# Optimization experiments

Hardware: AMD Instinct MI355X
Metric: run time of the kernel (lower is better)

Reference implementation:

```python
import jax, jax.numpy as jnp
import numpy as np

EPS = 1e-5      # BatchNorm eps (eval mode, running stats at init: mean=0, var=1)
SLOPE = 0.2     # LeakyReLU negative slope


def _knn_idx(x, k):
    # x: (B, N, D) -> (B, N, k) indices of k nearest neighbors (squared L2, feature space)
    sq = jnp.sum(x * x, axis=-1)                              # (B, N)
    dist = sq[:, :, None] + sq[:, None, :] - 2.0 * jnp.einsum('bnd,bmd->bnm', x, x)
    return jax.lax.top_k(-dist, k)[1]                         # nearest = largest of -dist


def _bn_lrelu(y, gamma, beta):
    # eval BatchNorm with running_mean=0, running_var=1, then LeakyReLU(0.2)
    y = y * (gamma / jnp.sqrt(1.0 + EPS)) + beta
    return jnp.where(y >= 0, y, SLOPE * y)


def _edge_conv(x, W, gamma, beta, k):
    # x: (B, N, D); W: (C_out, 2D). Returns (B, N, C_out) after max over k neighbors.
    idx = _knn_idx(x, k)                                      # (B, N, k)
    nb = jax.vmap(lambda xt, i: xt[i])(x, idx)                # (B, N, k, D) neighbor gather
    ctr = jnp.broadcast_to(x[:, :, None, :], nb.shape)
    feat = jnp.concatenate([nb - ctr, ctr], axis=-1)          # (B, N, k, 2D)
    y = jnp.einsum('bnkd,od->bnko', feat, W)                  # 1x1 conv (no bias)
    y = _bn_lrelu(y, gamma, beta)
    return jnp.max(y, axis=2)                                 # max-pool over neighbors


def setup_inputs() -> dict:
    key = jax.random.key(0)
    ks = jax.random.split(key, 16)
    B, N, k, out_dim = 8, 4096, 20, 512
    x = jax.random.normal(ks[0], (B, 3, N), dtype=jnp.float32)
    dims = [(64, 6), (64, 128), (128, 128), (256, 256), (out_dim, 512)]
    inp = {'x': x, 'k': k}
    for i, (co, ci) in enumerate(dims, start=1):
        inp[f'W{i}'] = jax.random.normal(ks[3 * i - 2], (co, ci), dtype=jnp.float32) * (1.0 / np.sqrt(ci))
        inp[f'g{i}'] = jax.random.uniform(ks[3 * i - 1], (co,), dtype=jnp.float32, minval=0.5, maxval=1.5)
        inp[f'b{i}'] = 0.1 * jax.random.normal(ks[3 * i], (co,), dtype=jnp.float32)
    return inp


def reference(x, W1, g1, b1, W2, g2, b2, W3, g3, b3, W4, g4, b4, W5, g5, b5, k):
    xt = jnp.transpose(x, (0, 2, 1))                          # (B, N, 3)
    x1 = _edge_conv(xt, W1, g1, b1, k)                        # (B, N, 64)
    x2 = _edge_conv(x1, W2, g2, b2, k)                        # (B, N, 64)
    x3 = _edge_conv(x2, W3, g3, b3, k)                        # (B, N, 128)
    x4 = _edge_conv(x3, W4, g4, b4, k)                        # (B, N, 256)
    h = jnp.concatenate([x1, x2, x3, x4], axis=-1)            # (B, N, 512)
    y = _bn_lrelu(jnp.einsum('bnd,od->bno', h, W5), g5, b5)   # (B, N, out_dim)
    return jnp.concatenate([jnp.max(y, axis=1), jnp.mean(y, axis=1)], axis=-1)  # (B, 2*out_dim)
```

## Files before the change

### kernel.cpp

```cpp
#include <hip/hip_runtime.h>
#include <math.h>

#define BATCH 8
#define N_PTS 4096
#define KNN 20
#define EPS_BN 1e-5f
#define SLOPE 0.2f
#define M_ROWS (BATCH * N_PTS)

typedef __attribute__((ext_vector_type(8))) short short8;
typedef __attribute__((ext_vector_type(2))) float float2v;
typedef __attribute__((ext_vector_type(4))) float float4v;
typedef __attribute__((ext_vector_type(16))) float float16v;

__device__ __forceinline__ unsigned short f2bf(float f) {
    unsigned u = __float_as_uint(f);
    unsigned r = (u + 0x7FFFu + ((u >> 16) & 1u)) >> 16;
    return (unsigned short)r;
}
__device__ __forceinline__ float bf2f(unsigned short h) {
    return __uint_as_float((unsigned)h << 16);
}

__global__ void convert_x1(const float* __restrict__ x,
                           unsigned short* __restrict__ xh, unsigned short* __restrict__ xl,
                           float* __restrict__ sq) {
    int i = blockIdx.x * blockDim.x + threadIdx.x;
    if (i >= M_ROWS) return;
    int b = i / N_PTS, n = i % N_PTS;
    float v[3], s = 0.f;
    #pragma unroll
    for (int d = 0; d < 3; ++d) {
        v[d] = x[((size_t)b * 3 + d) * N_PTS + n];
        s += v[d] * v[d];
    }
    sq[i] = s;
    #pragma unroll
    for (int d = 0; d < 32; ++d) {
        float f = (d < 3) ? v[d] : 0.f;
        unsigned short h = f2bf(f);
        xh[(size_t)i * 32 + d] = h;
        xl[(size_t)i * 32 + d] = f2bf(f - bf2f(h));
    }
}

__global__ void sqnorm_hl(const unsigned short* __restrict__ hh,
                          const unsigned short* __restrict__ hl,
                          int D, float* __restrict__ sq) {
    int w = threadIdx.x >> 6, lane = threadIdx.x & 63;
    int row = blockIdx.x * 4 + w;
    if (row >= M_ROWS) return;
    const unsigned short* ph = hh + (size_t)row * 512;
    const unsigned short* pl = hl + (size_t)row * 512;
    float s = 0.f;
    for (int d = lane; d < D; d += 64) {
        float v = bf2f(ph[d]) + bf2f(pl[d]);
        s += v * v;
    }
    #pragma unroll
    for (int off = 32; off > 0; off >>= 1) s += __shfl_down(s, off, 64);
    if (lane == 0) sq[row] = s;
}

__global__ void repack_edge_split(const float* __restrict__ W, int Co, int D, int KP,
                                  unsigned short* __restrict__ Wh, unsigned short* __restrict__ Wl) {
    int i = blockIdx.x * blockDim.x + threadIdx.x;
    int tot = 2 * Co * KP;
    if (i >= tot) return;
    int r = i / KP, d = i % KP;
    float v = 0.f;
    if (d < D) v = (r < Co) ? W[(size_t)r * 2 * D + d] : W[(size_t)(r - Co) * 2 * D + D + d];
    unsigned short h = f2bf(v);
    Wh[i] = h; Wl[i] = f2bf(v - bf2f(h));
}

__global__ void repack_w5_split(const float* __restrict__ W,
                                unsigned short* __restrict__ Wh, unsigned short* __restrict__ Wl) {
    int i = blockIdx.x * blockDim.x + threadIdx.x;
    if (i >= 512 * 512) return;
    float v = W[i];
    unsigned short h = f2bf(v);
    Wh[i] = h; Wl[i] = f2bf(v - bf2f(h));
}

template<int DPAD>
__launch_bounds__(256, 2)
__global__ void knn_mfma(const unsigned short* __restrict__ Xh,
                         const unsigned short* __restrict__ Xl,
                         int strideX,
                         const float* __restrict__ sq, int* __restrict__ idxout) {
    constexpr int KS16 = DPAD / 16;
    constexpr bool PF  = (KS16 <= 4);
    constexpr int SST  = 34;
    constexpr size_t SFB   = (size_t)4 * 32 * SST * 4;
    constexpr size_t MERGE = (size_t)64 * 4 * KNN * 4 * 2;
    constexpr size_t POOL  = (SFB + 256 * 4) > MERGE ? (SFB + 256 * 4) : MERGE;
    __shared__ __align__(16) char smem[POOL];
    float* Sfw  = (float*)smem + (size_t)(threadIdx.x >> 6) * 32 * SST;
    float* thrT = (float*)smem + (size_t)4 * 32 * SST;
    float*    kb = (float*)smem;
    unsigned* ib = (unsigned*)(kb + 64 * 4 * KNN);

    const int b = blockIdx.y;
    const int row0 = blockIdx.x * 64;
    const int tid = threadIdx.x;
    const int w = tid >> 6, lane = tid & 63;
    const int l31 = lane & 31, lh = lane >> 5;
    const int rbase = (w & 1) * 32;
    const int cb32  = (w >> 1) * 32;
    const int rowb  = rbase + l31;
    const int slot  = (w >> 1) * 2 + lh;

    const unsigned short* Xhb = Xh + (size_t)b * N_PTS * strideX;
    const unsigned short* Xlb = Xl + (size_t)b * N_PTS * strideX;
    const float* sqb = sq + (size_t)b * N_PTS;

    short8 ah[KS16], al[KS16];
    #pragma unroll
    for (int ks = 0; ks < KS16; ++ks) {
        size_t o = (size_t)(row0 + rbase + l31) * strideX + ks * 16 + lh * 8;
        ah[ks] = *(const short8*)(Xhb + o);
        al[ks] = *(const short8*)(Xlb + o);
    }

    const unsigned short* pBh = Xhb + (size_t)(cb32 + l31) * strideX + lh * 8;
    const unsigned short* pBl = Xlb + (size_t)(cb32 + l31) * strideX + lh * 8;
    const float* psq = sqb + cb32 + l31;

    float fv[KNN]; int fi[KNN];
    #pragma unroll
    for (int p = 0; p < KNN; ++p) { fv[p] = INFINITY; fi[p] = 0x7FFFFFFF; }

    thrT[tid] = INFINITY;
    __syncthreads();

    short8 bhA[KS16], blA[KS16], bhB[KS16], blB[KS16];
    if constexpr (PF) {
        #pragma unroll
        for (int ks = 0; ks < KS16; ++ks) {
            bhA[ks] = *(const short8*)(pBh + ks * 16);
            blA[ks] = *(const short8*)(pBl + ks * 16);
        }
    }

    auto body = [&](short8 (&bch)[KS16], short8 (&bcl)[KS16],
                    short8 (&bnh)[KS16], short8 (&bnl)[KS16], int c0) {
        if constexpr (!PF) {
            #pragma unroll
            for (int ks = 0; ks < KS16; ++ks) {
                bch[ks] = *(const short8*)(pBh + (size_t)c0 * strideX + ks * 16);
                bcl[ks] = *(const short8*)(pBl + (size_t)c0 * strideX + ks * 16);
            }
        } else {
            int cp = (c0 + 64 < N_PTS) ? c0 + 64 : 0;
            #pragma unroll
            for (int ks = 0; ks < KS16; ++ks) {
                bnh[ks] = *(const short8*)(pBh + (size_t)cp * strideX + ks * 16);
                bnl[ks] = *(const short8*)(pBl + (size_t)cp * strideX + ks * 16);
            }
        }
        float sc = psq[c0];

        float16v a0 = {}, a1 = {}, a2 = {};
        #pragma unroll
        for (int ks = 0; ks < KS16; ++ks) {
            if constexpr (PF) {
                a0 = __builtin_amdgcn_mfma_f32_32x32x16_bf16(ah[ks], bch[ks], a0, 0, 0, 0);
                a1 = __builtin_amdgcn_mfma_f32_32x32x16_bf16(al[ks], bch[ks], a1, 0, 0, 0);
                a2 = __builtin_amdgcn_mfma_f32_32x32x16_bf16(ah[ks], bcl[ks], a2, 0, 0, 0);
            } else {
                a0 = __builtin_amdgcn_mfma_f32_32x32x16_bf16(ah[ks], bch[ks], a0, 0, 0, 0);
                a1 = __builtin_amdgcn_mfma_f32_32x32x16_bf16(al[ks], bch[ks], a1, 0, 0, 0);
                a0 = __builtin_amdgcn_mfma_f32_32x32x16_bf16(ah[ks], bcl[ks], a0, 0, 0, 0);
            }
        }

        #pragma unroll
        for (int reg = 0; reg < 16; ++reg) {
            int rowL = (reg & 3) + 8 * (reg >> 2) + 4 * lh;
            float acv = PF ? (a0[reg] + a1[reg] + a2[reg]) : (a0[reg] + a1[reg]);
            Sfw[rowL * SST + l31] = sc - 2.f * acv;
        }
        asm volatile("s_waitcnt lgkmcnt(0)" ::: "memory");

        float fT = fminf(fminf(thrT[rowb], thrT[64 + rowb]),
                         fminf(thrT[128 + rowb], thrT[192 + rowb]));
        float f19 = fv[KNN - 1];

        const int sbase = l31 * SST + lh * 16;
        float2v c2[8];
        #pragma unroll
        for (int u = 0; u < 8; ++u) c2[u] = *(const float2v*)&Sfw[sbase + 2 * u];
        unsigned mask = 0;
        #pragma unroll
        for (int u = 0; u < 8; ++u) {
            if (c2[u][0] < f19 && c2[u][0] <= fT) mask |= (1u << (2 * u));
            if (c2[u][1] < f19 && c2[u][1] <= fT) mask |= (1u << (2 * u + 1));
        }

        const int cidx = c0 + cb32 + lh * 16;
        while (mask) {
            int jj = __ffs(mask) - 1;
            mask &= mask - 1;
            bool j1 = jj & 1, j2 = jj & 2, j4 = jj & 4, j8 = jj & 8;
            float t0 = j1 ? c2[0][1] : c2[0][0];
            float t1 = j1 ? c2[1][1] : c2[1][0];
            float t2 = j1 ? c2[2][1] : c2[2][0];
            float t3 = j1 ? c2[3][1] : c2[3][0];
            float t4 = j1 ? c2[4][1] : c2[4][0];
            float t5 = j1 ? c2[5][1] : c2[5][0];
            float t6 = j1 ? c2[6][1] : c2[6][0];
            float t7 = j1 ? c2[7][1] : c2[7][0];
            float u0 = j2 ? t1 : t0;
            float u1 = j2 ? t3 : t2;
            float u2 = j2 ? t5 : t4;
            float u3 = j2 ? t7 : t6;
            float r0 = j4 ? u1 : u0;
            float r1 = j4 ? u3 : u2;
            float v  = j8 ? r1 : r0;
            if (v < fv[KNN - 1]) {
                fv[KNN - 1] = v;
                fi[KNN - 1] = cidx + jj;
                #pragma unroll
                for (int p = KNN - 1; p > 0; --p) {
                    float va = fv[p - 1], vb = fv[p];
                    int   ia = fi[p - 1], ic = fi[p];
                    bool sw = vb < va;
                    fv[p - 1] = sw ? vb : va; fv[p] = sw ? va : vb;
                    fi[p - 1] = sw ? ic : ia; fi[p] = sw ? ia : ic;
                }
            }
        }

        thrT[slot * 64 + rowb] = fv[KNN - 1];
    };

    #pragma unroll 1
    for (int c0 = 0; c0 < N_PTS; c0 += 128) {
        body(bhA, blA, bhB, blB, c0);
        body(bhB, blB, bhA, blA, c0 + 64);
    }

    __syncthreads();
    {
        int base = (rowb * 4 + slot) * KNN;
        #pragma unroll
        for (int p = 0; p < KNN; ++p) { kb[base + p] = fv[p]; ib[base + p] = (unsigned)fi[p]; }
    }
    __syncthreads();
    if (tid < 64) {
        int base = tid * 4 * KNN;
        #pragma unroll
        for (int p = 0; p < KNN; ++p) { fv[p] = kb[base + p]; fi[p] = (int)ib[base + p]; }
        #pragma unroll 1
        for (int qq = 0; qq < 3 * KNN; ++qq) {
            float    v  = kb[base + KNN + qq];
            unsigned ii = ib[base + KNN + qq];
            bool ins = (v < fv[KNN - 1]) ||
                       (v == fv[KNN - 1] && (int)ii < fi[KNN - 1]);
            if (ins) {
                fv[KNN - 1] = v; fi[KNN - 1] = (int)ii;
                #pragma unroll
                for (int p = KNN - 1; p > 0; --p) {
                    float va = fv[p - 1], vb = fv[p];
                    int   ia = fi[p - 1], ic = fi[p];
                    bool sw = (vb < va) || (vb == va && ic < ia);
                    fv[p - 1] = sw ? vb : va; fv[p] = sw ? va : vb;
                    fi[p - 1] = sw ? ic : ia; fi[p] = sw ? ia : ic;
                }
            }
        }
        int* op = idxout + ((size_t)(b * N_PTS + row0 + tid)) * KNN;
        #pragma unroll
        for (int p = 0; p < KNN; ++p) op[p] = fi[p];
    }
}

__launch_bounds__(256)
__global__ void fgemm(const unsigned short* __restrict__ Ah, const unsigned short* __restrict__ Al,
                      int strideA, int K,
                      const unsigned short* __restrict__ Wh, const unsigned short* __restrict__ Wl,
                      int C, float* __restrict__ out, int fuse_bn,
                      const float* __restrict__ g, const float* __restrict__ beta) {
    __shared__ unsigned short AhS[128 * 40];
    __shared__ unsigned short AlS[128 * 40];
    __shared__ unsigned short BhS[128 * 40];
    __shared__ unsigned short BlS[128 * 40];

    const int c0 = blockIdx.x * 128;
    const int m0 = blockIdx.y * 128;
    const int tid = threadIdx.x;
    const int w = tid >> 6, lane = tid & 63;
    const int n = lane & 15, q = lane >> 4;

    float4v acc[2][8];
    #pragma unroll
    for (int rt = 0; rt < 2; ++rt)
        #pragma unroll
        for (int ct = 0; ct < 8; ++ct) acc[rt][ct] = (float4v){0.f, 0.f, 0.f, 0.f};

    for (int kk = 0; kk < K; kk += 32) {
        __syncthreads();
        for (int tt = tid; tt < 512; tt += 256) {
            int rr = tt >> 2, c8 = tt & 3;
            size_t oa = (size_t)(m0 + rr) * strideA + kk + c8 * 8;
            *(short8*)&AhS[rr * 40 + c8 * 8] = *(const short8*)(Ah + oa);
            *(short8*)&AlS[rr * 40 + c8 * 8] = *(const short8*)(Al + oa);
            size_t ob = (size_t)(c0 + rr) * K + kk + c8 * 8;
            *(short8*)&BhS[rr * 40 + c8 * 8] = *(const short8*)(Wh + ob);
            *(short8*)&BlS[rr * 40 + c8 * 8] = *(const short8*)(Wl + ob);
        }
        __syncthreads();

        short8 af[2][2];
        #pragma unroll
        for (int rt = 0; rt < 2; ++rt) {
            af[rt][0] = *(const short8*)&AhS[(w * 32 + rt * 16 + n) * 40 + q * 8];
            af[rt][1] = *(const short8*)&AlS[(w * 32 + rt * 16 + n) * 40 + q * 8];
        }
        #pragma unroll
        for (int ct = 0; ct < 8; ++ct) {
            short8 bh = *(const short8*)&BhS[(ct * 16 + n) * 40 + q * 8];
            short8 bl = *(const short8*)&BlS[(ct * 16 + n) * 40 + q * 8];
            #pragma unroll
            for (int rt = 0; rt < 2; ++rt) {
                acc[rt][ct] = __builtin_amdgcn_mfma_f32_16x16x32_bf16(af[rt][0], bh, acc[rt][ct], 0, 0, 0);
                acc[rt][ct] = __builtin_amdgcn_mfma_f32_16x16x32_bf16(af[rt][1], bh, acc[rt][ct], 0, 0, 0);
                acc[rt][ct] = __builtin_amdgcn_mfma_f32_16x16x32_bf16(af[rt][0], bl, acc[rt][ct], 0, 0, 0);
            }
        }
    }

    #pragma unroll
    for (int rt = 0; rt < 2; ++rt)
        #pragma unroll
        for (int ct = 0; ct < 8; ++ct) {
            int c = c0 + ct * 16 + n;
            float sc = 1.f, bt = 0.f;
            if (fuse_bn) { sc = g[c] / sqrtf(1.f + EPS_BN); bt = beta[c]; }
            #pragma unroll
            for (int e = 0; e < 4; ++e) {
                int m = m0 + w * 32 + rt * 16 + q * 4 + e;
                float v = acc[rt][ct][e];
                if (fuse_bn) { v = v * sc + bt; v = (v >= 0.f) ? v : SLOPE * v; }
                out[(size_t)m * C + c] = v;
            }
        }
}

__global__ void pool_kernel(const float* __restrict__ zc2, int Co,
                            const int* __restrict__ idx,
                            const float* __restrict__ g, const float* __restrict__ beta,
                            unsigned short* __restrict__ hh, unsigned short* __restrict__ hl,
                            int hoff) {
    int n = blockIdx.x, b = blockIdx.y;
    int o = threadIdx.x;
    size_t bn = (size_t)b * N_PTS + n;
    const int* ip = idx + bn * KNN;
    float zn   = zc2[bn * (size_t)(2 * Co) + o];
    float base = zc2[bn * (size_t)(2 * Co) + Co + o] - zn;
    float m = -INFINITY;
    #pragma unroll
    for (int j = 0; j < KNN; ++j) {
        size_t rr = (size_t)b * N_PTS + ip[j];
        m = fmaxf(m, zc2[rr * (size_t)(2 * Co) + o]);
    }
    float y = m + base;
    float sc = g[o] / sqrtf(1.f + EPS_BN);
    y = y * sc + beta[o];
    y = (y >= 0.f) ? y : SLOPE * y;
    unsigned short h = f2bf(y);
    hh[bn * 512 + hoff + o] = h;
    hl[bn * 512 + hoff + o] = f2bf(y - bf2f(h));
}

__global__ void reduce_partial(const float* __restrict__ y5,
                               float* __restrict__ pmax, float* __restrict__ psum) {
    int chunk = blockIdx.x, b = blockIdx.y, c = threadIdx.x;
    float mx = -INFINITY, sm = 0.f;
    for (int qq = 0; qq < 128; ++qq) {
        int n = chunk * 128 + qq;
        float v = y5[((size_t)b * N_PTS + n) * 512 + c];
        mx = fmaxf(mx, v);
        sm += v;
    }
    pmax[((size_t)b * 32 + chunk) * 512 + c] = mx;
    psum[((size_t)b * 32 + chunk) * 512 + c] = sm;
}

__global__ void reduce_final(const float* __restrict__ pmax,
                             const float* __restrict__ psum,
                             float* __restrict__ out) {
    int i = blockIdx.x * blockDim.x + threadIdx.x;
    if (i >= BATCH * 512) return;
    int b = i / 512, c = i % 512;
    float mx = -INFINITY, sm = 0.f;
    for (int qq = 0; qq < 32; ++qq) {
        mx = fmaxf(mx, pmax[((size_t)b * 32 + qq) * 512 + c]);
        sm += psum[((size_t)b * 32 + qq) * 512 + c];
    }
    out[(size_t)b * 1024 + c] = mx;
    out[(size_t)b * 1024 + 512 + c] = sm * (1.f / 4096.f);
}

extern "C" void kernel_launch(void* const* d_in, const int* in_sizes, int n_in,
                              void* d_out, int out_size, void* d_ws, size_t ws_size,
                              hipStream_t stream) {
    const float* x = (const float*)d_in[0];
    const float* W[5], *gg[5], *bb[5];
    for (int i = 0; i < 5; ++i) {
        W[i]  = (const float*)d_in[2 + 3 * i];
        gg[i] = (const float*)d_in[3 + 3 * i];
        bb[i] = (const float*)d_in[4 + 3 * i];
    }
    float* outp = (float*)d_out;

    char* wsb = (char*)d_ws;
    size_t off = 0;
    unsigned short* x1h = (unsigned short*)(wsb + off); off += (size_t)M_ROWS * 32 * 2;
    unsigned short* x1l = (unsigned short*)(wsb + off); off += (size_t)M_ROWS * 32 * 2;
    float* sq = (float*)(wsb + off); off += (size_t)M_ROWS * 4;
    int*   idx = (int*)(wsb + off); off += (size_t)M_ROWS * KNN * 4;
    unsigned short* Wh = (unsigned short*)(wsb + off); off += (size_t)512 * 512 * 2;
    unsigned short* Wl = (unsigned short*)(wsb + off); off += (size_t)512 * 512 * 2;
    unsigned short* hh = (unsigned short*)(wsb + off); off += (size_t)M_ROWS * 512 * 2;
    unsigned short* hl = (unsigned short*)(wsb + off); off += (size_t)M_ROWS * 512 * 2;
    float* zc2 = (float*)(wsb + off); off += (size_t)M_ROWS * 512 * 4;
    float* pmx = (float*)(wsb + off); off += (size_t)BATCH * 32 * 512 * 4;
    float* psm = (float*)(wsb + off); off += (size_t)BATCH * 32 * 512 * 4;
    (void)ws_size; (void)in_sizes; (void)n_in; (void)out_size;

    convert_x1<<<(M_ROWS + 255) / 256, 256, 0, stream>>>(x, x1h, x1l, sq);

    struct L { int D, Co, KP, hoff; };
    const L layers[4] = { {3, 64, 32, 0}, {64, 64, 64, 64}, {64, 128, 64, 128}, {128, 256, 128, 256} };

    for (int li = 0; li < 4; ++li) {
        const L& ly = layers[li];
        const unsigned short* Ahp;
        const unsigned short* Alp;
        int strideA;
        if (li == 0) { Ahp = x1h; Alp = x1l; strideA = 32; }
        else {
            int po = layers[li - 1].hoff;
            Ahp = hh + po; Alp = hl + po; strideA = 512;
            sqnorm_hl<<<M_ROWS / 4, 256, 0, stream>>>(Ahp, Alp, ly.D, sq);
        }

        if (li == 0)
            knn_mfma<32><<<dim3(N_PTS / 64, BATCH), 256, 0, stream>>>(Ahp, Alp, strideA, sq, idx);
        else if (ly.D == 64)
            knn_mfma<64><<<dim3(N_PTS / 64, BATCH), 256, 0, stream>>>(Ahp, Alp, strideA, sq, idx);
        else
            knn_mfma<128><<<dim3(N_PTS / 64, BATCH), 256, 0, stream>>>(Ahp, Alp, strideA, sq, idx);

        repack_edge_split<<<(2 * ly.Co * ly.KP + 255) / 256, 256, 0, stream>>>(
            W[li], ly.Co, ly.D, ly.KP, Wh, Wl);
        fgemm<<<dim3((2 * ly.Co) / 128, M_ROWS / 128), 256, 0, stream>>>(
            Ahp, Alp, strideA, ly.KP, Wh, Wl, 2 * ly.Co, zc2, 0, nullptr, nullptr);
        pool_kernel<<<dim3(N_PTS, BATCH), ly.Co, 0, stream>>>(
            zc2, ly.Co, idx, gg[li], bb[li], hh, hl, ly.hoff);
    }

    repack_w5_split<<<(512 * 512 + 255) / 256, 256, 0, stream>>>(W[4], Wh, Wl);
    fgemm<<<dim3(4, M_ROWS / 128), 256, 0, stream>>>(
        hh, hl, 512, 512, Wh, Wl, 512, zc2, 1, gg[4], bb[4]);

    reduce_partial<<<dim3(32, BATCH), 512, 0, stream>>>(zc2, pmx, psm);
    reduce_final<<<(BATCH * 512 + 255) / 256, 256, 0, stream>>>(pmx, psm, outp);
}
```

Before: 1.500 ms.

## Split KNN column range across 8 waves for low-dim layers with two-stage merge

For the D=32/64 KNN kernels, the block grows to 512 threads (8 waves), and each half of the waves scans half of the candidate columns. The per-slot top-k lists are then merged in two stages. Candidate indices in the merge buffer are stored as 16-bit values to keep shared memory small enough for 4 blocks per CU. This is meant to raise parallelism and latency hiding for the serial candidate scan, at the cost of a larger merge phase, an extra barrier and more register pressure under the tighter launch bounds.

```diff
diff --git a/kernel.cpp b/kernel.cpp
--- a/kernel.cpp
+++ b/kernel.cpp
@@ -84,22 +84,26 @@
 }
 
 template<int DPAD>
-__launch_bounds__(256, 2)
+__launch_bounds__(DPAD >= 128 ? 256 : 512, DPAD >= 128 ? 2 : 4)
 __global__ void knn_mfma(const unsigned short* __restrict__ Xh,
                          const unsigned short* __restrict__ Xl,
                          int strideX,
                          const float* __restrict__ sq, int* __restrict__ idxout) {
     constexpr int KS16 = DPAD / 16;
     constexpr bool PF  = (KS16 <= 4);
+    constexpr int NW   = (DPAD >= 128) ? 4 : 8;
+    constexpr int NCH  = NW / 4;
+    constexpr int CHR  = N_PTS / NCH;
     constexpr int SST  = 34;
-    constexpr size_t SFB   = (size_t)4 * 32 * SST * 4;
-    constexpr size_t MERGE = (size_t)64 * 4 * KNN * 4 * 2;
-    constexpr size_t POOL  = (SFB + 256 * 4) > MERGE ? (SFB + 256 * 4) : MERGE;
+    constexpr size_t SFB   = (size_t)NW * 32 * SST * 4;
+    constexpr size_t THR   = (size_t)NW * 64 * 4;
+    constexpr size_t MERGE = (size_t)64 * NW * KNN * 4 + (size_t)64 * NW * KNN * 2;
+    constexpr size_t POOL  = (SFB + THR) > MERGE ? (SFB + THR) : MERGE;
     __shared__ __align__(16) char smem[POOL];
     float* Sfw  = (float*)smem + (size_t)(threadIdx.x >> 6) * 32 * SST;
-    float* thrT = (float*)smem + (size_t)4 * 32 * SST;
-    float*    kb = (float*)smem;
-    unsigned* ib = (unsigned*)(kb + 64 * 4 * KNN);
+    float* thrT = (float*)(smem + SFB);
+    float*          kb   = (float*)smem;
+    unsigned short* ib16 = (unsigned short*)(kb + 64 * NW * KNN);
 
     const int b = blockIdx.y;
     const int row0 = blockIdx.x * 64;
@@ -107,9 +111,11 @@
     const int w = tid >> 6, lane = tid & 63;
     const int l31 = lane & 31, lh = lane >> 5;
     const int rbase = (w & 1) * 32;
-    const int cb32  = (w >> 1) * 32;
+    const int cb32  = ((w >> 1) & 1) * 32;
+    const int chalf = w >> 2;
+    const int cs    = chalf * CHR;
     const int rowb  = rbase + l31;
-    const int slot  = (w >> 1) * 2 + lh;
+    const int slot  = ((w >> 1) & 1) * 2 + lh + chalf * 4;
 
     const unsigned short* Xhb = Xh + (size_t)b * N_PTS * strideX;
     const unsigned short* Xlb = Xl + (size_t)b * N_PTS * strideX;
@@ -138,8 +144,8 @@
     if constexpr (PF) {
         #pragma unroll
         for (int ks = 0; ks < KS16; ++ks) {
-            bhA[ks] = *(const short8*)(pBh + ks * 16);
-            blA[ks] = *(const short8*)(pBl + ks * 16);
+            bhA[ks] = *(const short8*)(pBh + (size_t)cs * strideX + ks * 16);
+            blA[ks] = *(const short8*)(pBl + (size_t)cs * strideX + ks * 16);
         }
     }
 
@@ -152,7 +158,7 @@
                 bcl[ks] = *(const short8*)(pBl + (size_t)c0 * strideX + ks * 16);
             }
         } else {
-            int cp = (c0 + 64 < N_PTS) ? c0 + 64 : 0;
+            int cp = (c0 + 64 < cs + CHR) ? c0 + 64 : cs;
             #pragma unroll
             for (int ks = 0; ks < KS16; ++ks) {
                 bnh[ks] = *(const short8*)(pBh + (size_t)cp * strideX + ks * 16);
@@ -183,8 +189,9 @@
         }
         asm volatile("s_waitcnt lgkmcnt(0)" ::: "memory");
 
-        float fT = fminf(fminf(thrT[rowb], thrT[64 + rowb]),
-                         fminf(thrT[128 + rowb], thrT[192 + rowb]));
+        float fT = thrT[rowb];
+        #pragma unroll
+        for (int s = 1; s < NW; ++s) fT = fminf(fT, thrT[s * 64 + rowb]);
         float f19 = fv[KNN - 1];
 
         const int sbase = l31 * SST + lh * 16;
@@ -235,44 +242,113 @@
         thrT[slot * 64 + rowb] = fv[KNN - 1];
     };
 
-    #pragma unroll 1
-    for (int c0 = 0; c0 < N_PTS; c0 += 128) {
-        body(bhA, blA, bhB, blB, c0);
-        body(bhB, blB, bhA, blA, c0 + 64);
+    if constexpr (PF) {
+        #pragma unroll 1
+        for (int c0 = cs; c0 < cs + CHR; c0 += 128) {
+            body(bhA, blA, bhB, blB, c0);
+            body(bhB, blB, bhA, blA, c0 + 64);
+        }
+    } else {
+        #pragma unroll 1
+        for (int c0 = cs; c0 < cs + CHR; c0 += 64)
+            body(bhA, blA, bhB, blB, c0);
     }
 
     __syncthreads();
     {
-        int base = (rowb * 4 + slot) * KNN;
-        #pragma unroll
-        for (int p = 0; p < KNN; ++p) { kb[base + p] = fv[p]; ib[base + p] = (unsigned)fi[p]; }
+        int base = (rowb * NW + slot) * KNN;
+        #pragma unroll
+        for (int p = 0; p < KNN; ++p) {
+            kb[base + p] = fv[p];
+            ib16[base + p] = (unsigned short)fi[p];
+        }
     }
     __syncthreads();
-    if (tid < 64) {
-        int base = tid * 4 * KNN;
-        #pragma unroll
-        for (int p = 0; p < KNN; ++p) { fv[p] = kb[base + p]; fi[p] = (int)ib[base + p]; }
-        #pragma unroll 1
-        for (int qq = 0; qq < 3 * KNN; ++qq) {
-            float    v  = kb[base + KNN + qq];
-            unsigned ii = ib[base + KNN + qq];
-            bool ins = (v < fv[KNN - 1]) ||
-                       (v == fv[KNN - 1] && (int)ii < fi[KNN - 1]);
-            if (ins) {
-                fv[KNN - 1] = v; fi[KNN - 1] = (int)ii;
+
+    if constexpr (NW == 8) {
+        if (tid < 128) {
+            int row = tid & 63, half = tid >> 6;
+            int base = (row * 8 + half * 4) * KNN;
+            #pragma unroll
+            for (int p = 0; p < KNN; ++p) { fv[p] = kb[base + p]; fi[p] = (int)ib16[base + p]; }
+            #pragma unroll 1
+            for (int qq = 0; qq < 3 * KNN; ++qq) {
+                float v  = kb[base + KNN + qq];
+                int   ii = (int)ib16[base + KNN + qq];
+                bool ins = (v < fv[KNN - 1]) ||
+                           (v == fv[KNN - 1] && ii < fi[KNN - 1]);
+                if (ins) {
+                    fv[KNN - 1] = v; fi[KNN - 1] = ii;
+                    #pragma unroll
+                    for (int p = KNN - 1; p > 0; --p) {
+                        float va = fv[p - 1], vb = fv[p];
+                        int   ia = fi[p - 1], ic = fi[p];
+                        bool sw = (vb < va) || (vb == va && ic < ia);
+                        fv[p - 1] = sw ? vb : va; fv[p] = sw ? va : vb;
+                        fi[p - 1] = sw ? ic : ia; fi[p] = sw ? ia : ic;
+                    }
+                }
+            }
+            if (half == 1) {
+                int ob = (row * 8 + 4) * KNN;
                 #pragma unroll
-                for (int p = KNN - 1; p > 0; --p) {
-                    float va = fv[p - 1], vb = fv[p];
-                    int   ia = fi[p - 1], ic = fi[p];
-                    bool sw = (vb < va) || (vb == va && ic < ia);
-                    fv[p - 1] = sw ? vb : va; fv[p] = sw ? va : vb;
-                    fi[p - 1] = sw ? ic : ia; fi[p] = sw ? ia : ic;
+                for (int p = 0; p < KNN; ++p) {
+                    kb[ob + p] = fv[p]; ib16[ob + p] = (unsigned short)fi[p];
                 }
             }
         }
-        int* op = idxout + ((size_t)(b * N_PTS + row0 + tid)) * KNN;
-        #pragma unroll
-        for (int p = 0; p < KNN; ++p) op[p] = fi[p];
+        __syncthreads();
+        if (tid < 64) {
+            int base = (tid * 8 + 4) * KNN;
+            #pragma unroll 1
+            for (int qq = 0; qq < KNN; ++qq) {
+                float v  = kb[base + qq];
+                int   ii = (int)ib16[base + qq];
+                bool ins = (v < fv[KNN - 1]) ||
+                           (v == fv[KNN - 1] && ii < fi[KNN - 1]);
+                if (ins) {
+                    fv[KNN - 1] = v; fi[KNN - 1] = ii;
+                    #pragma unroll
+                    for (int p = KNN - 1; p > 0; --p) {
+                        float va = fv[p - 1], vb = fv[p];
+                        int   ia = fi[p - 1], ic = fi[p];
+                        bool sw = (vb < va) || (vb == va && ic < ia);
+                        fv[p - 1] = sw ? vb : va; fv[p] = sw ? va : vb;
+                        fi[p - 1] = sw ? ic : ia; fi[p] = sw ? ia : ic;
+                    }
+                }
+            }
+            int* op = idxout + ((size_t)(b * N_PTS + row0 + tid)) * KNN;
+            #pragma unroll
+            for (int p = 0; p < KNN; ++p) op[p] = fi[p];
+        }
+    } else {
+        if (tid < 64) {
+            int base = tid * 4 * KNN;
+            #pragma unroll
+            for (int p = 0; p < KNN; ++p) { fv[p] = kb[base + p]; fi[p] = (int)ib16[base + p]; }
+            #pragma unroll 1
+            for (int qq = 0; qq < 3 * KNN; ++qq) {
+                float v  = kb[base + KNN + qq];
+                int   ii = (int)ib16[base + KNN + qq];
+                bool ins = (v < fv[KNN - 1]) ||
+                           (v == fv[KNN - 1] && ii < fi[KNN - 1]);
+                if (ins) {
+                    fv[KNN - 1] = v; fi[KNN - 1] = ii;
+                    #pragma unroll
+                    for (int p = KNN - 1; p > 0; --p) {
+                        float va = fv[p - 1], vb = fv[p];
+                        int   ia = fi[p - 1], ic = fi[p];
+                        bool sw = (vb < va) || (vb == va && ic < ia);
+                        fv[p - 1] = sw ? vb : va; fv[p] = sw ? va : vb;
+                        fi[p - 1] = sw ? ic : ia; fi[p] = sw ? ia : ic;
+                    }
+                }
+            }
+            int* op = idxout + ((size_t)(b * N_PTS + row0 + tid)) * KNN;
+            #pragma unroll
+            for (int p = 0; p < KNN; ++p) op[p] = fi[p];
+        }
     }
 }
 
@@ -448,9 +524,9 @@
         }
 
         if (li == 0)
-            knn_mfma<32><<<dim3(N_PTS / 64, BATCH), 256, 0, stream>>>(Ahp, Alp, strideA, sq, idx);
+            knn_mfma<32><<<dim3(N_PTS / 64, BATCH), 512, 0, stream>>>(Ahp, Alp, strideA, sq, idx);
         else if (ly.D == 64)
-            knn_mfma<64><<<dim3(N_PTS / 64, BATCH), 256, 0, stream>>>(Ahp, Alp, strideA, sq, idx);
+            knn_mfma<64><<<dim3(N_PTS / 64, BATCH), 512, 0, stream>>>(Ahp, Alp, strideA, sq, idx);
         else
             knn_mfma<128><<<dim3(N_PTS / 64, BATCH), 256, 0, stream>>>(Ahp, Alp, strideA, sq, idx);
 
```

New measurement: 1.724 ms. 14.9% more time.
